# Performance work log

Measured on AMD Instinct MI355X. Metric: run time of the kernel, lower is better.

Reference implementation:

```python
import jax, jax.numpy as jnp
import numpy as np

B, T, C = 2, 2048, 2048
N, K, H = 16, 4, 128      # heads, kv heads, head dim
G = N // K                # query groups per kv head
ROPE_THETA = 10000.0
N_LAYERS = 24
SOFTCAP = 50.0


def _sine_table(features, length, max_timescale):
    fraction = jnp.arange(0, features, 2, dtype=jnp.float32) / features
    timescale = max_timescale ** fraction  # min_timescale = 1.0
    sinusoid = jnp.einsum('i,j->ij', jnp.arange(length, dtype=jnp.float32),
                          1.0 / timescale, precision=jax.lax.Precision.HIGHEST)
    sinusoid = jnp.concatenate([sinusoid, sinusoid], axis=-1)  # (length, features)
    return jnp.sin(sinusoid), jnp.cos(sinusoid)


def _rotate_half(x):
    x1, x2 = jnp.split(x, 2, axis=-1)
    return jnp.concatenate([-x2, x1], axis=-1)


def setup_inputs() -> dict:
    key = jax.random.key(0)
    kx, kq, kk, kv, ko = jax.random.split(key, 5)
    init_std = np.sqrt(2.0 / (5.0 * C)).astype(np.float32)
    wang_std = np.float32(2.0 / N_LAYERS / np.sqrt(N * H))
    return {
        'x': jax.random.normal(kx, (B, T, C), dtype=jnp.float32),
        'q_kernel': jax.random.normal(kq, (C, N * H), dtype=jnp.float32) * init_std,
        'k_kernel': jax.random.normal(kk, (C, K * H), dtype=jnp.float32) * init_std,
        'v_kernel': jax.random.normal(kv, (C, K * H), dtype=jnp.float32) * init_std,
        'out_kernel': jax.random.normal(ko, (N * H, C), dtype=jnp.float32) * wang_std,
    }


def reference(x, q_kernel, k_kernel, v_kernel, out_kernel):
    q = jnp.dot(x, q_kernel).reshape(B, T, K, G, H)
    k = jnp.dot(x, k_kernel).reshape(B, T, K, H)
    v = jnp.dot(x, v_kernel).reshape(B, T, K, H)

    # RoPE (note original passes cos into the `sin` slot and vice versa by name,
    # but the computation uses cos with identity part and sin with rotate_half).
    sin, cos = _sine_table(H, T, ROPE_THETA)
    qcos = cos[None, :, None, None, :]  # (1,T,1,1,H)
    qsin = sin[None, :, None, None, :]
    kcos = cos[None, :, None, :]        # (1,T,1,H)
    ksin = sin[None, :, None, :]
    q = q * qcos + _rotate_half(q) * qsin
    k = k * kcos + _rotate_half(k) * ksin

    scale = jax.lax.rsqrt(jnp.float32(H))
    logits = jnp.einsum('btkgh,bskh->bkgts', q * scale, k)  # (B,K,G,T,S)
    logits = jnp.tanh(logits / SOFTCAP) * SOFTCAP
    causal = jnp.tril(jnp.ones((T, T), dtype=jnp.bool_))
    neg = jnp.asarray(-0.7 * jnp.finfo(logits.dtype).max, dtype=logits.dtype)
    logits = jnp.where(causal[None, None, None, :, :], logits, neg)
    probs = jax.nn.softmax(logits.astype(jnp.float32), axis=-1).astype(logits.dtype)
    encoded = jnp.einsum('bkgts,bskh->btkgh', probs, v)
    encoded = encoded.reshape(B, T, N * H)
    return jnp.dot(encoded, out_kernel)
```

## Files before the change

### kernel.cpp

```cpp
#include <hip/hip_runtime.h>
#include <stdint.h>

typedef unsigned short u16;
typedef __bf16 bf16x8 __attribute__((ext_vector_type(8)));
typedef float f32x4 __attribute__((ext_vector_type(4)));

#define T_SEQ 2048
#define KVH 4

__device__ __forceinline__ u16 f2b(float f) {
  uint32_t u = __builtin_bit_cast(uint32_t, f);
  u += 0x7FFFu + ((u >> 16) & 1u);
  return (u16)(u >> 16);
}
__device__ __forceinline__ float b2f(u16 h) {
  uint32_t u = ((uint32_t)h) << 16;
  return __builtin_bit_cast(float, u);
}

__device__ __forceinline__ void gload16(const void* g, void* l) {
  __builtin_amdgcn_global_load_lds((const __attribute__((address_space(1))) void*)g,
                                   (__attribute__((address_space(3))) void*)l, 16, 0, 0);
}

__global__ void k_f32_to_bf16(const float* __restrict__ in, u16* __restrict__ out, int n4) {
  int i = blockIdx.x * blockDim.x + threadIdx.x;
  if (i >= n4) return;
  float4 v = reinterpret_cast<const float4*>(in)[i];
  ushort4 o;
  o.x = f2b(v.x); o.y = f2b(v.y); o.z = f2b(v.z); o.w = f2b(v.w);
  reinterpret_cast<ushort4*>(out)[i] = o;
}

__global__ void k_transpose_f32_bf16(const float* __restrict__ in, u16* __restrict__ out,
                                     int R, int Cc) {
  __shared__ float tile[32][33];
  const int c0 = blockIdx.x * 32, r0 = blockIdx.y * 32;
  const int tx = threadIdx.x, ty = threadIdx.y;
  for (int i = ty; i < 32; i += 8) tile[i][tx] = in[(size_t)(r0 + i) * Cc + c0 + tx];
  __syncthreads();
  for (int i = ty; i < 32; i += 8) out[(size_t)(c0 + i) * R + r0 + tx] = f2b(tile[tx][i]);
}

template <int OUT_BF16>
__global__ __launch_bounds__(256, 2) void k_gemm(const u16* __restrict__ A,
                                                 const u16* __restrict__ Bt,
                                                 void* __restrict__ Cp,
                                                 int M, int N, int Kd,
                                                 int lda, int ldb, int ldc) {
  __align__(16) __shared__ u16 As[128 * 32];
  __align__(16) __shared__ u16 Bs[128 * 32];
  const int tid = threadIdx.x;
  const int wid = tid >> 6, lane = tid & 63;
  const int lg = lane >> 4, lm = lane & 15;
  const int bm = blockIdx.x, bn = blockIdx.y;
  const int wr = wid >> 1, wc = wid & 1;

  const int srow = wid * 32 + (lane >> 2);
  const int scol = (lane & 3) * 8;
  const u16* ap0 = A + (size_t)(bm * 128 + srow) * lda + scol;
  const u16* ap1 = ap0 + (size_t)16 * lda;
  const u16* bp0 = Bt + (size_t)(bn * 128 + srow) * ldb + scol;
  const u16* bp1 = bp0 + (size_t)16 * ldb;
  u16* asDst0 = As + wid * 1024;
  u16* asDst1 = As + wid * 1024 + 512;
  u16* bsDst0 = Bs + wid * 1024;
  u16* bsDst1 = Bs + wid * 1024 + 512;

  const f32x4 z4 = {0.f, 0.f, 0.f, 0.f};
  f32x4 acc[4][4];
#pragma unroll
  for (int i = 0; i < 4; ++i)
#pragma unroll
    for (int j = 0; j < 4; ++j) acc[i][j] = z4;

  const int nk = Kd >> 5;
  for (int kb = 0; kb < nk; ++kb) {
    gload16(ap0, asDst0);
    gload16(ap1, asDst1);
    gload16(bp0, bsDst0);
    gload16(bp1, bsDst1);
    ap0 += 32; ap1 += 32; bp0 += 32; bp1 += 32;
    __syncthreads();
    bf16x8 af[4], bfr[4];
#pragma unroll
    for (int i = 0; i < 4; ++i)
      af[i] = *(const bf16x8*)(As + (wr * 64 + i * 16 + lm) * 32 + lg * 8);
#pragma unroll
    for (int j = 0; j < 4; ++j)
      bfr[j] = *(const bf16x8*)(Bs + (wc * 64 + j * 16 + lm) * 32 + lg * 8);
#pragma unroll
    for (int i = 0; i < 4; ++i)
#pragma unroll
      for (int j = 0; j < 4; ++j)
        acc[i][j] = __builtin_amdgcn_mfma_f32_16x16x32_bf16(af[i], bfr[j], acc[i][j], 0, 0, 0);
    __syncthreads();
  }

#pragma unroll
  for (int i = 0; i < 4; ++i) {
    const int row = bm * 128 + wr * 64 + i * 16 + lg * 4;
#pragma unroll
    for (int j = 0; j < 4; ++j) {
      const int col = bn * 128 + wc * 64 + j * 16 + lm;
#pragma unroll
      for (int r = 0; r < 4; ++r) {
        const float v = acc[i][j][r];
        if (OUT_BF16)
          ((u16*)Cp)[(size_t)(row + r) * ldc + col] = f2b(v);
        else
          ((float*)Cp)[(size_t)(row + r) * ldc + col] = v;
      }
    }
  }
}

__global__ void k_rope_q(const u16* __restrict__ qkv, u16* __restrict__ qbf) {
  const int idx = blockIdx.x * 256 + threadIdx.x;
  const int j = idx & 63;
  const int n = (idx >> 6) & 15;
  const int m = idx >> 10;
  const int t = m & (T_SEQ - 1);
  const float inv = __expf((float)j * -0.14391157f);
  const float ang = (float)t * inv;
  float s, c;
  __sincosf(ang, &s, &c);
  const u16* row = qkv + (size_t)m * 3072 + n * 128;
  const float x1 = b2f(row[j]), x2 = b2f(row[j + 64]);
  const float scale = 0.08838834764831845f;
  u16* orow = qbf + (size_t)m * 2048 + n * 128;
  orow[j] = f2b((x1 * c - x2 * s) * scale);
  orow[j + 64] = f2b((x2 * c + x1 * s) * scale);
}

__global__ void k_rope_k(const u16* __restrict__ qkv, u16* __restrict__ kbf) {
  const int idx = blockIdx.x * 256 + threadIdx.x;
  const int j = idx & 63;
  const int kh = (idx >> 6) & 3;
  const int m = idx >> 8;
  const int t = m & (T_SEQ - 1);
  const int b = m >> 11;
  const float inv = __expf((float)j * -0.14391157f);
  const float ang = (float)t * inv;
  float s, c;
  __sincosf(ang, &s, &c);
  const u16* row = qkv + (size_t)m * 3072 + 2048 + kh * 128;
  const float x1 = b2f(row[j]), x2 = b2f(row[j + 64]);
  u16* orow = kbf + ((size_t)(b * KVH + kh) * T_SEQ + t) * 128;
  orow[j] = f2b(x1 * c - x2 * s);
  orow[j + 64] = f2b(x2 * c + x1 * s);
}

__global__ void k_v_transpose(const u16* __restrict__ qkv, u16* __restrict__ vt) {
  __shared__ u16 tile[32][33];
  const int t0 = blockIdx.x * 32, h0 = blockIdx.y * 32, bk = blockIdx.z;
  const int b = bk >> 2, kh = bk & 3;
  const int tx = threadIdx.x, ty = threadIdx.y;
  for (int i = ty; i < 32; i += 8)
    tile[i][tx] = qkv[(size_t)(b * T_SEQ + t0 + i) * 3072 + 2560 + kh * 128 + h0 + tx];
  __syncthreads();
  for (int i = ty; i < 32; i += 8)
    vt[(size_t)bk * (128 * T_SEQ) + (size_t)(h0 + i) * T_SEQ + t0 + tx] = tile[tx][i];
}

__global__ __launch_bounds__(256, 2) void k_attn(const u16* __restrict__ qbf,
                                                 const u16* __restrict__ kbf,
                                                 const u16* __restrict__ vt,
                                                 u16* __restrict__ enc) {
  __shared__ __align__(16) u16 smem[36864];
  u16* const Ks0 = smem;
  u16* const Vs0 = smem + 16384;

  const int n = blockIdx.y, b = blockIdx.z;
  const int qt = (b == 0) ? (15 - blockIdx.x) : blockIdx.x;
  const int kh = n >> 2;
  const int tid = threadIdx.x;
  const int wid = tid >> 6;
  const int lane = tid & 63;
  const int lg = lane >> 4;
  const int lm = lane & 15;
  const int q0w = qt * 128 + wid * 32;
  u16* const Pl = smem + 32768 + wid * 1024;

  bf16x8 qfA[4], qfB[4];
  {
    const u16* qrowA = qbf + (size_t)(b * T_SEQ + q0w + lm) * 2048 + n * 128 + lg * 8;
    const u16* qrowB = qrowA + 16 * 2048;
#pragma unroll
    for (int c = 0; c < 4; ++c) {
      qfA[c] = *(const bf16x8*)(qrowA + c * 32);
      qfB[c] = *(const bf16x8*)(qrowB + c * 32);
    }
  }
  const u16* const kg = kbf + (size_t)(b * KVH + kh) * T_SEQ * 128;
  const u16* const vg = vt + (size_t)(b * KVH + kh) * 128 * T_SEQ;

  const int swz = lm & 7;
  int koff[4], voff[2], poff[4];
#pragma unroll
  for (int c = 0; c < 4; ++c) koff[c] = lm * 128 + (((c * 4 + lg) ^ swz) * 8);
#pragma unroll
  for (int ks = 0; ks < 2; ++ks) voff[ks] = lm * 64 + (((ks * 4 + lg) ^ swz) * 8);
#pragma unroll
  for (int st = 0; st < 4; ++st)
    poff[st] = lm * 64 + (((st * 2 + (lg >> 1)) ^ swz) * 8) + (lg & 1) * 4;

  const f32x4 z4 = {0.f, 0.f, 0.f, 0.f};
  f32x4 accA[8], accB[8];
#pragma unroll
  for (int h = 0; h < 8; ++h) { accA[h] = z4; accB[h] = z4; }
  float lA = 0.f, lB = 0.f;

  const int ntiles = 2 * qt + 2;

  auto STAGE = [&](int buf, int kb2) {
    const int kv2 = kb2 * 64;
    const u16* ksrc = kg + (size_t)kv2 * 128;
    u16* kdst = Ks0 + buf * 8192;
    u16* vdst = Vs0 + buf * 8192;
#pragma unroll
    for (int i = 0; i < 4; ++i) {
      const int g = tid + i * 256;
      const int row = g >> 4, u = g & 15;
      gload16(ksrc + row * 128 + ((u ^ (row & 7)) * 8), kdst + g * 8);
    }
#pragma unroll
    for (int i = 0; i < 4; ++i) {
      const int g = tid + i * 256;
      const int row = g >> 3, u = g & 7;
      gload16(vg + (size_t)row * T_SEQ + kv2 + ((u ^ (row & 7)) * 8), vdst + g * 8);
    }
  };

  auto tile_p = [&](f32x4* sa, float& lsum, bf16x8* pf, int tg, bool needMask, int kv) {
    float p[16];
#pragma unroll
    for (int st = 0; st < 4; ++st)
#pragma unroll
      for (int r = 0; r < 4; ++r) p[st * 4 + r] = sa[st][r];
#pragma unroll
    for (int i = 0; i < 16; ++i) {
      const float e = __builtin_amdgcn_exp2f(p[i] * 0.05770780163555853f);
      p[i] = __builtin_amdgcn_exp2f(-144.269504088896f * __builtin_amdgcn_rcpf(e + 1.f));
    }
    if (needMask) {
#pragma unroll
      for (int i = 0; i < 16; ++i) {
        const int sg = kv + (i >> 2) * 16 + lg * 4 + (i & 3);
        if (sg > tg) p[i] = 0.f;
      }
    }
#pragma unroll
    for (int i = 0; i < 16; ++i) lsum += p[i];
#pragma unroll
    for (int st = 0; st < 4; ++st) {
      ushort4 w4;
      w4.x = f2b(p[st * 4 + 0]);
      w4.y = f2b(p[st * 4 + 1]);
      w4.z = f2b(p[st * 4 + 2]);
      w4.w = f2b(p[st * 4 + 3]);
      *(ushort4*)(Pl + poff[st]) = w4;
    }
    asm volatile("s_waitcnt lgkmcnt(0)" ::: "memory");
#pragma unroll
    for (int ks = 0; ks < 2; ++ks) pf[ks] = *(const bf16x8*)(Pl + voff[ks]);
  };

  STAGE(0, 0);
  asm volatile("s_waitcnt vmcnt(0)" ::: "memory");
  __syncthreads();

  for (int kb = 0; kb < ntiles; ++kb) {
    const int cur = kb & 1;
    if (kb + 1 < ntiles) STAGE(cur ^ 1, kb + 1);
    const int kv = kb * 64;
    if (kv <= q0w + 31) {
      const u16* KsC = Ks0 + cur * 8192;
      const u16* VsC = Vs0 + cur * 8192;

      f32x4 saA[4] = {z4, z4, z4, z4};
      f32x4 saB[4] = {z4, z4, z4, z4};
      __builtin_amdgcn_s_setprio(1);
#pragma unroll
      for (int st = 0; st < 4; ++st) {
#pragma unroll
        for (int c = 0; c < 4; ++c) {
          const bf16x8 kf = *(const bf16x8*)(KsC + st * 2048 + koff[c]);
          saA[st] = __builtin_amdgcn_mfma_f32_16x16x32_bf16(kf, qfA[c], saA[st], 0, 0, 0);
          saB[st] = __builtin_amdgcn_mfma_f32_16x16x32_bf16(kf, qfB[c], saB[st], 0, 0, 0);
        }
      }
      __builtin_amdgcn_s_setprio(0);

      bf16x8 pfA[2], pfB[2];
      tile_p(saA, lA, pfA, q0w + lm, kv + 63 > q0w, kv);
      tile_p(saB, lB, pfB, q0w + 16 + lm, kv + 63 > q0w + 16, kv);

      __builtin_amdgcn_s_setprio(1);
#pragma unroll
      for (int h = 0; h < 8; ++h) {
#pragma unroll
        for (int ks = 0; ks < 2; ++ks) {
          const bf16x8 vf = *(const bf16x8*)(VsC + h * 1024 + voff[ks]);
          accA[h] = __builtin_amdgcn_mfma_f32_16x16x32_bf16(pfA[ks], vf, accA[h], 0, 0, 0);
          accB[h] = __builtin_amdgcn_mfma_f32_16x16x32_bf16(pfB[ks], vf, accB[h], 0, 0, 0);
        }
      }
      __builtin_amdgcn_s_setprio(0);
    }
    asm volatile("s_waitcnt vmcnt(0)" ::: "memory");
    __syncthreads();
  }

  lA += __shfl_xor(lA, 16); lA += __shfl_xor(lA, 32);
  lB += __shfl_xor(lB, 16); lB += __shfl_xor(lB, 32);
  float liA[4], liB[4];
#pragma unroll
  for (int r = 0; r < 4; ++r) {
    liA[r] = 1.f / __shfl(lA, lg * 4 + r);
    liB[r] = 1.f / __shfl(lB, lg * 4 + r);
  }
#pragma unroll
  for (int h = 0; h < 8; ++h) {
#pragma unroll
    for (int r = 0; r < 4; ++r) {
      const size_t colo = n * 128 + h * 16 + lm;
      enc[(size_t)(b * T_SEQ + q0w + lg * 4 + r) * 2048 + colo] = f2b(accA[h][r] * liA[r]);
      enc[(size_t)(b * T_SEQ + q0w + 16 + lg * 4 + r) * 2048 + colo] = f2b(accB[h][r] * liB[r]);
    }
  }
}

extern "C" void kernel_launch(void* const* d_in, const int* in_sizes, int n_in,
                              void* d_out, int out_size, void* d_ws, size_t ws_size,
                              hipStream_t stream) {
  const float* x  = (const float*)d_in[0];
  const float* wq = (const float*)d_in[1];
  const float* wk = (const float*)d_in[2];
  const float* wv = (const float*)d_in[3];
  const float* wo = (const float*)d_in[4];

  char* ws = (char*)d_ws;
  u16* x_bf  = (u16*)(ws);
  u16* wqkvt = (u16*)(ws + 16777216);
  u16* wot   = (u16*)(ws + 29360128);
  u16* qkv   = (u16*)(ws + 37748736);
  u16* enc   = qkv;
  u16* q_bf  = (u16*)(ws + 62914560);
  u16* k_bf  = (u16*)(ws + 79691776);
  u16* vt    = (u16*)(ws + 83886080);
  if (ws_size < 88080384) return;
  (void)in_sizes; (void)n_in; (void)out_size;

  k_f32_to_bf16<<<dim3(8192), dim3(256), 0, stream>>>(x, x_bf, 8388608 / 4);
  k_transpose_f32_bf16<<<dim3(64, 64), dim3(32, 8), 0, stream>>>(wq, wqkvt, 2048, 2048);
  k_transpose_f32_bf16<<<dim3(16, 64), dim3(32, 8), 0, stream>>>(wk, wqkvt + 2048 * 2048, 2048, 512);
  k_transpose_f32_bf16<<<dim3(16, 64), dim3(32, 8), 0, stream>>>(wv, wqkvt + 2560 * 2048, 2048, 512);
  k_transpose_f32_bf16<<<dim3(64, 64), dim3(32, 8), 0, stream>>>(wo, wot, 2048, 2048);
  k_gemm<1><<<dim3(32, 24), dim3(256), 0, stream>>>(x_bf, wqkvt, qkv,
                                                    4096, 3072, 2048, 2048, 2048, 3072);
  k_rope_q<<<dim3(16384), dim3(256), 0, stream>>>(qkv, q_bf);
  k_rope_k<<<dim3(4096), dim3(256), 0, stream>>>(qkv, k_bf);
  k_v_transpose<<<dim3(64, 4, 8), dim3(32, 8), 0, stream>>>(qkv, vt);
  k_attn<<<dim3(16, 16, 2), dim3(256), 0, stream>>>(q_bf, k_bf, vt, enc);
  k_gemm<0><<<dim3(32, 16), dim3(256), 0, stream>>>(enc, wot, d_out,
                                                    4096, 2048, 2048, 2048, 2048, 2048);
}
```

Baseline: 215.5 us.

## Split attention KV loop across two wave halves with LDS reduction

The attention kernel now uses 512 threads per block. Two groups of four waves each take alternating 64-key tiles, so each block stages two KV tiles per iteration and makes half as many loop trips. At the end, the second half writes its partial accumulators and row sums to shared memory, and the first half adds them before normalizing and storing. The aim is more waves per block to hide latency and a shorter serial KV loop, at the cost of doubled LDS use, one block per CU, and an extra reduction pass. Because the softmax does not subtract a running max, partial sums can be added directly.

```diff
diff --git a/kernel.cpp b/kernel.cpp
--- a/kernel.cpp
+++ b/kernel.cpp
@@ -163,24 +163,24 @@
     vt[(size_t)bk * (128 * T_SEQ) + (size_t)(h0 + i) * T_SEQ + t0 + tx] = tile[tx][i];
 }
 
-__global__ __launch_bounds__(256, 2) void k_attn(const u16* __restrict__ qbf,
+__global__ __launch_bounds__(512, 1) void k_attn(const u16* __restrict__ qbf,
                                                  const u16* __restrict__ kbf,
                                                  const u16* __restrict__ vt,
                                                  u16* __restrict__ enc) {
-  __shared__ __align__(16) u16 smem[36864];
-  u16* const Ks0 = smem;
-  u16* const Vs0 = smem + 16384;
+  __shared__ __align__(16) u16 smem[73728];
 
   const int n = blockIdx.y, b = blockIdx.z;
   const int qt = (b == 0) ? (15 - blockIdx.x) : blockIdx.x;
   const int kh = n >> 2;
   const int tid = threadIdx.x;
   const int wid = tid >> 6;
+  const int half = wid >> 2;
+  const int wq = wid & 3;
   const int lane = tid & 63;
   const int lg = lane >> 4;
   const int lm = lane & 15;
-  const int q0w = qt * 128 + wid * 32;
-  u16* const Pl = smem + 32768 + wid * 1024;
+  const int q0w = qt * 128 + wq * 32;
+  u16* const Pl = smem + 65536 + wid * 1024;
 
   bf16x8 qfA[4], qfB[4];
   {
@@ -211,24 +211,25 @@
   for (int h = 0; h < 8; ++h) { accA[h] = z4; accB[h] = z4; }
   float lA = 0.f, lB = 0.f;
 
-  const int ntiles = 2 * qt + 2;
-
-  auto STAGE = [&](int buf, int kb2) {
-    const int kv2 = kb2 * 64;
-    const u16* ksrc = kg + (size_t)kv2 * 128;
-    u16* kdst = Ks0 + buf * 8192;
-    u16* vdst = Vs0 + buf * 8192;
-#pragma unroll
-    for (int i = 0; i < 4; ++i) {
-      const int g = tid + i * 256;
-      const int row = g >> 4, u = g & 15;
-      gload16(ksrc + row * 128 + ((u ^ (row & 7)) * 8), kdst + g * 8);
-    }
-#pragma unroll
-    for (int i = 0; i < 4; ++i) {
-      const int g = tid + i * 256;
-      const int row = g >> 3, u = g & 7;
-      gload16(vg + (size_t)row * T_SEQ + kv2 + ((u ^ (row & 7)) * 8), vdst + g * 8);
+  auto STAGE = [&](int buf, int j2) {
+#pragma unroll
+    for (int hh = 0; hh < 2; ++hh) {
+      const int kv2 = (2 * j2 + hh) * 64;
+      const u16* ksrc = kg + (size_t)kv2 * 128;
+      u16* kdst = smem + (hh * 2 + buf) * 8192;
+      u16* vdst = smem + 32768 + (hh * 2 + buf) * 8192;
+#pragma unroll
+      for (int i = 0; i < 2; ++i) {
+        const int g = tid + i * 512;
+        const int row = g >> 4, u = g & 15;
+        gload16(ksrc + row * 128 + ((u ^ (row & 7)) * 8), kdst + g * 8);
+      }
+#pragma unroll
+      for (int i = 0; i < 2; ++i) {
+        const int g = tid + i * 512;
+        const int row = g >> 3, u = g & 7;
+        gload16(vg + (size_t)row * T_SEQ + kv2 + ((u ^ (row & 7)) * 8), vdst + g * 8);
+      }
     }
   };
 
@@ -270,13 +271,13 @@
   asm volatile("s_waitcnt vmcnt(0)" ::: "memory");
   __syncthreads();
 
-  for (int kb = 0; kb < ntiles; ++kb) {
-    const int cur = kb & 1;
-    if (kb + 1 < ntiles) STAGE(cur ^ 1, kb + 1);
-    const int kv = kb * 64;
+  for (int j = 0; j <= qt; ++j) {
+    const int cur = j & 1;
+    if (j < qt) STAGE(cur ^ 1, j + 1);
+    const int kv = (2 * j + half) * 64;
     if (kv <= q0w + 31) {
-      const u16* KsC = Ks0 + cur * 8192;
-      const u16* VsC = Vs0 + cur * 8192;
+      const u16* KsC = smem + (half * 2 + cur) * 8192;
+      const u16* VsC = smem + 32768 + (half * 2 + cur) * 8192;
 
       f32x4 saA[4] = {z4, z4, z4, z4};
       f32x4 saB[4] = {z4, z4, z4, z4};
@@ -312,21 +313,49 @@
     __syncthreads();
   }
 
-  lA += __shfl_xor(lA, 16); lA += __shfl_xor(lA, 32);
-  lB += __shfl_xor(lB, 16); lB += __shfl_xor(lB, 32);
-  float liA[4], liB[4];
-#pragma unroll
-  for (int r = 0; r < 4; ++r) {
-    liA[r] = 1.f / __shfl(lA, lg * 4 + r);
-    liB[r] = 1.f / __shfl(lB, lg * 4 + r);
-  }
-#pragma unroll
-  for (int h = 0; h < 8; ++h) {
+  float* const scrO = (float*)smem;
+  float* const scrL = (float*)smem + 16384;
+  if (half == 1) {
+    float* w = scrO + wq * 4096 + lane;
+#pragma unroll
+    for (int h = 0; h < 8; ++h)
+#pragma unroll
+      for (int r = 0; r < 4; ++r) {
+        w[(h * 4 + r) * 64] = accA[h][r];
+        w[(32 + h * 4 + r) * 64] = accB[h][r];
+      }
+    scrL[wq * 128 + lane * 2] = lA;
+    scrL[wq * 128 + lane * 2 + 1] = lB;
+  }
+  __syncthreads();
+  if (half == 0) {
+    const float* w = scrO + wq * 4096 + lane;
+#pragma unroll
+    for (int h = 0; h < 8; ++h)
+#pragma unroll
+      for (int r = 0; r < 4; ++r) {
+        accA[h][r] += w[(h * 4 + r) * 64];
+        accB[h][r] += w[(32 + h * 4 + r) * 64];
+      }
+    lA += scrL[wq * 128 + lane * 2];
+    lB += scrL[wq * 128 + lane * 2 + 1];
+
+    lA += __shfl_xor(lA, 16); lA += __shfl_xor(lA, 32);
+    lB += __shfl_xor(lB, 16); lB += __shfl_xor(lB, 32);
+    float liA[4], liB[4];
 #pragma unroll
     for (int r = 0; r < 4; ++r) {
-      const size_t colo = n * 128 + h * 16 + lm;
-      enc[(size_t)(b * T_SEQ + q0w + lg * 4 + r) * 2048 + colo] = f2b(accA[h][r] * liA[r]);
-      enc[(size_t)(b * T_SEQ + q0w + 16 + lg * 4 + r) * 2048 + colo] = f2b(accB[h][r] * liB[r]);
+      liA[r] = 1.f / __shfl(lA, lg * 4 + r);
+      liB[r] = 1.f / __shfl(lB, lg * 4 + r);
+    }
+#pragma unroll
+    for (int h = 0; h < 8; ++h) {
+#pragma unroll
+      for (int r = 0; r < 4; ++r) {
+        const size_t colo = n * 128 + h * 16 + lm;
+        enc[(size_t)(b * T_SEQ + q0w + lg * 4 + r) * 2048 + colo] = f2b(accA[h][r] * liA[r]);
+        enc[(size_t)(b * T_SEQ + q0w + 16 + lg * 4 + r) * 2048 + colo] = f2b(accB[h][r] * liB[r]);
+      }
     }
   }
 }
@@ -362,7 +391,7 @@
   k_rope_q<<<dim3(16384), dim3(256), 0, stream>>>(qkv, q_bf);
   k_rope_k<<<dim3(4096), dim3(256), 0, stream>>>(qkv, k_bf);
   k_v_transpose<<<dim3(64, 4, 8), dim3(32, 8), 0, stream>>>(qkv, vt);
-  k_attn<<<dim3(16, 16, 2), dim3(256), 0, stream>>>(q_bf, k_bf, vt, enc);
+  k_attn<<<dim3(16, 16, 2), dim3(512), 0, stream>>>(q_bf, k_bf, vt, enc);
   k_gemm<0><<<dim3(32, 16), dim3(256), 0, stream>>>(enc, wot, d_out,
                                                     4096, 2048, 2048, 2048, 2048, 2048);
 }
```

New measurement: 231.2 us. 7.3% more time.
